# Performance work log

Hardware: AMD Instinct MI355X
Metric: run time of the kernel (lower is better)

The kernel has to match this reference:

```python
import jax, jax.numpy as jnp
import numpy as np

B, S, D, H = 2, 2048, 1024, 16
DK = D // H

def setup_inputs() -> dict:
    key = jax.random.key(0)
    ks = jax.random.split(key, 11)
    def lin(kw, kb):
        # torch nn.Linear init scale ~ 1/sqrt(fan_in)
        s = 1.0 / np.sqrt(D)
        W = jax.random.uniform(kw, (D, D), jnp.float32, -s, s)
        b = jax.random.uniform(kb, (D,), jnp.float32, -s, s)
        return W, b
    Wq, bq = lin(ks[0], ks[1])
    Wk, bk = lin(ks[2], ks[3])
    Wv, bv = lin(ks[4], ks[5])
    Wo, bo = lin(ks[6], ks[7])
    query = jax.random.normal(ks[8], (B, S, D), jnp.float32)
    key_t = jax.random.normal(ks[9], (B, S, D), jnp.float32)
    value = jax.random.normal(ks[10], (B, S, D), jnp.float32)
    return {"query": query, "key": key_t, "value": value,
            "Wq": Wq, "bq": bq, "Wk": Wk, "bk": bk,
            "Wv": Wv, "bv": bv, "Wo": Wo, "bo": bo}

def reference(query, key, value, Wq, bq, Wk, bk, Wv, bv, Wo, bo):
    # linear projections (torch Linear: x @ W.T + b), split heads -> (B,H,S,DK)
    def proj(x, W, b):
        y = jnp.einsum('bsd,ed->bse', x, W) + b
        return y.reshape(B, -1, H, DK).transpose(0, 2, 1, 3)
    q = proj(query, Wq, bq)
    k = proj(key, Wk, bk)
    v = proj(value, Wv, bv)
    # scaled dot-product attention, full score matrix (B,H,Sq,Sk)
    scores = jnp.einsum('bhqd,bhkd->bhqk', q, k) / jnp.sqrt(jnp.float32(DK))
    attn = jax.nn.softmax(scores, axis=-1)
    ctx = jnp.einsum('bhqk,bhkd->bhqd', attn, v)
    # merge heads and output projection; dropout is identity in eval mode
    ctx = ctx.transpose(0, 2, 1, 3).reshape(B, -1, D)
    out = jnp.einsum('bsd,ed->bse', ctx, Wo) + bo
    attn_weights = attn.mean(axis=1)  # average_weights=True -> (B,Sq,Sk)
    return (out, attn_weights)
```

## Files before the change

### kernel.cpp

```cpp
#include <hip/hip_runtime.h>

#define B_ 2
#define S_ 2048
#define D_ 1024
#define H_ 16
#define DK_ 64
#define M_ (B_ * S_)

typedef __bf16 bf16;
typedef __attribute__((ext_vector_type(8))) __bf16 bf16x8;
typedef __attribute__((ext_vector_type(4))) __bf16 bf16x4;
typedef __attribute__((ext_vector_type(4))) float f32x4;

static __device__ __forceinline__ bf16x8 ld8(const bf16* p) {
    return *(const bf16x8*)p;
}

static __device__ __forceinline__ void g2l16(const void* g, void* l) {
    __builtin_amdgcn_global_load_lds(
        (const __attribute__((address_space(1))) unsigned int*)g,
        (__attribute__((address_space(3))) unsigned int*)l, 16, 0, 0);
}

__global__ __launch_bounds__(256)
void cvt_all(const float* __restrict__ xq, const float* __restrict__ xk,
             const float* __restrict__ xv, const float* __restrict__ wq,
             const float* __restrict__ wk, const float* __restrict__ wv,
             const float* __restrict__ wo, bf16* __restrict__ xqo,
             bf16* __restrict__ xko, bf16* __restrict__ xvo,
             bf16* __restrict__ wqo, bf16* __restrict__ wko,
             bf16* __restrict__ wvo, bf16* __restrict__ woo)
{
    const int bx = blockIdx.x;
    const float* s; bf16* d; size_t base;
    if (bx < 6144) {
        int a = bx >> 11;
        s = (a == 0) ? xq : (a == 1) ? xk : xv;
        d = (a == 0) ? xqo : (a == 1) ? xko : xvo;
        base = (size_t)(bx & 2047) * 2048;
    } else {
        int a = (bx - 6144) >> 9;
        s = (a == 0) ? wq : (a == 1) ? wk : (a == 2) ? wv : wo;
        d = (a == 0) ? wqo : (a == 1) ? wko : (a == 2) ? wvo : woo;
        base = (size_t)((bx - 6144) & 511) * 2048;
    }
    size_t i = base + (size_t)threadIdx.x * 8;
    f32x4 a4 = *(const f32x4*)(s + i);
    f32x4 b4 = *(const f32x4*)(s + i + 4);
    bf16x8 r;
    r[0]=(bf16)a4[0]; r[1]=(bf16)a4[1]; r[2]=(bf16)a4[2]; r[3]=(bf16)a4[3];
    r[4]=(bf16)b4[0]; r[5]=(bf16)b4[1]; r[6]=(bf16)b4[2]; r[7]=(bf16)b4[3];
    *(bf16x8*)(d + i) = r;
}

__global__ __launch_bounds__(256)
void gemm128(const bf16* __restrict__ A, const bf16* __restrict__ W,
             const float* __restrict__ bias, void* __restrict__ out,
             int a_headsplit, int out_mode, float scale)
{
    const int m0 = blockIdx.x * 128, n0 = blockIdx.y * 128;
    const int tid = threadIdx.x;
    const int wv = tid >> 6, lane = tid & 63, quad = lane >> 4, l16 = lane & 15;
    const int wr = (wv >> 1) * 64, wc = (wv & 1) * 64;

    __shared__ bf16 As[128 * 32];
    __shared__ bf16 Bs[128 * 32];

    f32x4 acc[4][4];
#pragma unroll
    for (int i = 0; i < 4; ++i)
#pragma unroll
        for (int j = 0; j < 4; ++j) acc[i][j] = f32x4{0.f, 0.f, 0.f, 0.f};

    const int srow = tid >> 2;
    const int scol = (tid & 3) * 8;

    for (int k0 = 0; k0 < D_; k0 += 32) {
        bf16x8 av[2], bw[2];
#pragma unroll
        for (int c = 0; c < 2; ++c) {
            const int row = c * 64 + srow;
            const int k   = k0 + scol;
            const bf16* ap;
            if (a_headsplit) {
                int m = m0 + row, bb = m >> 11, ss = m & (S_ - 1);
                int hh = k >> 6, dd = k & (DK_ - 1);
                ap = A + (((size_t)(bb * H_ + hh) * S_ + ss) * DK_ + dd);
            } else {
                ap = A + (size_t)(m0 + row) * D_ + k;
            }
            av[c] = ld8(ap);
            bw[c] = ld8(W + (size_t)(n0 + row) * D_ + k);
        }
        __syncthreads();
#pragma unroll
        for (int c = 0; c < 2; ++c) {
            const int e = c * 2048 + tid * 8;
            *(bf16x8*)(As + e) = av[c];
            *(bf16x8*)(Bs + e) = bw[c];
        }
        __syncthreads();

        bf16x8 af[4], bfr[4];
#pragma unroll
        for (int i = 0; i < 4; ++i)
            af[i] = *(const bf16x8*)(As + (wr + i*16 + l16) * 32 + quad * 8);
#pragma unroll
        for (int j = 0; j < 4; ++j)
            bfr[j] = *(const bf16x8*)(Bs + (wc + j*16 + l16) * 32 + quad * 8);
#pragma unroll
        for (int i = 0; i < 4; ++i)
#pragma unroll
            for (int j = 0; j < 4; ++j)
                acc[i][j] = __builtin_amdgcn_mfma_f32_16x16x32_bf16(
                    af[i], bfr[j], acc[i][j], 0, 0, 0);
    }

#pragma unroll
    for (int i = 0; i < 4; ++i)
#pragma unroll
        for (int j = 0; j < 4; ++j) {
            const int nn = n0 + wc + j*16 + l16;
            const float bvv = bias[nn];
            const int mm0 = m0 + wr + i*16 + quad*4;
            if (out_mode == 2) {
                bf16x4 pk;
#pragma unroll
                for (int r = 0; r < 4; ++r)
                    pk[r] = (bf16)((acc[i][j][r] + bvv) * scale);
                int bb = mm0 >> 11, ss = mm0 & (S_ - 1);
                int hh = nn >> 6,  dd = nn & (DK_ - 1);
                *(bf16x4*)((bf16*)out +
                    ((size_t)(bb * H_ + hh) * DK_ + dd) * S_ + ss) = pk;
            } else {
#pragma unroll
                for (int r = 0; r < 4; ++r) {
                    const int mm = mm0 + r;
                    float v = (acc[i][j][r] + bvv) * scale;
                    if (out_mode == 1) {
                        ((float*)out)[(size_t)mm * D_ + nn] = v;
                    } else {
                        int bb = mm >> 11, ss = mm & (S_ - 1);
                        int hh = nn >> 6, dd = nn & (DK_ - 1);
                        ((bf16*)out)[((size_t)(bb * H_ + hh) * S_ + ss) * DK_ + dd] = (bf16)v;
                    }
                }
            }
        }
}

__global__ __launch_bounds__(256)
void attn_ctx(const bf16* __restrict__ Q, const bf16* __restrict__ K,
              const bf16* __restrict__ Vt, float* __restrict__ Li,
              bf16* __restrict__ ctxOut)
{
    const int bid = blockIdx.x;
    const int l   = (bid & 7) * 128 + (bid >> 3);
    const int q0  = (l & 31) * 64;
    const int h   = (l >> 5) & 15;
    const int b   = l >> 9;

    const int tid = threadIdx.x;
    const int wv = tid >> 6, lane = tid & 63, quad = lane >> 4, l16 = lane & 15;

    __shared__ bf16 Kl[2][2048];
    __shared__ bf16 Vl[2][2048];

    const size_t hb = (size_t)(b * H_ + h) * S_;
    const int qw = q0 + wv * 16;

    bf16x8 qf0, qf1;
    {
        const bf16* qrow = Q + (hb + qw + l16) * DK_;
        qf0 = ld8(qrow + quad*8);
        qf1 = ld8(qrow + 32 + quad*8);
    }
    const bf16* Kb  = K  + hb * DK_;
    const bf16* Vtb = Vt + hb * DK_;

    f32x4 cacc[4];
#pragma unroll
    for (int db = 0; db < 4; ++db) cacc[db] = f32x4{0.f,0.f,0.f,0.f};
    float lsum = 0.f;

    const int kj = wv*8 + (lane >> 3);
    const int koff = (((lane & 7) ^ (lane >> 3)) << 4);
    const int vd = wv*16 + (lane >> 2);
    const int voff = (((lane & 3) ^ ((lane >> 2) & 3)) << 4);

    const char* Kbc = (const char*)Kb;
    const char* Vbc = (const char*)Vtb;

#define STAGE(jc, buf)                                                       \
    do {                                                                     \
        g2l16(Kbc + ((size_t)(jc) * 32 + kj) * 128 + koff,                   \
              &Kl[buf][wv * 512]);                                           \
        g2l16(Vbc + (size_t)vd * (S_ * 2) + (size_t)(jc) * 64 + voff,        \
              &Vl[buf][wv * 512]);                                           \
    } while (0)

    STAGE(0, 0);
    __syncthreads();

    int cur = 0;
    const int swk = (l16 & 7) << 4;
    const int swv = (l16 & 3) << 4;
    for (int jc = 0; jc < 64; ++jc) {
        STAGE((jc + 1) & 63, cur ^ 1);

        const char* kb = (const char*)&Kl[cur][0];
        const char* vb = (const char*)&Vl[cur][0];
        bf16x8 kf0a = *(const bf16x8*)(kb + l16*128 + ((quad*16) ^ swk));
        bf16x8 kf0b = *(const bf16x8*)(kb + l16*128 + ((64 + quad*16) ^ swk));
        bf16x8 kf1a = *(const bf16x8*)(kb + (16+l16)*128 + ((quad*16) ^ swk));
        bf16x8 kf1b = *(const bf16x8*)(kb + (16+l16)*128 + ((64 + quad*16) ^ swk));

        f32x4 z0 = {0.f,0.f,0.f,0.f}, z1 = {0.f,0.f,0.f,0.f};
        z0 = __builtin_amdgcn_mfma_f32_16x16x32_bf16(kf0a, qf0, z0, 0, 0, 0);
        f32x4 s0 = __builtin_amdgcn_mfma_f32_16x16x32_bf16(kf0b, qf1, z0, 0, 0, 0);
        z1 = __builtin_amdgcn_mfma_f32_16x16x32_bf16(kf1a, qf0, z1, 0, 0, 0);
        f32x4 s1 = __builtin_amdgcn_mfma_f32_16x16x32_bf16(kf1b, qf1, z1, 0, 0, 0);

        float e0 = __builtin_amdgcn_exp2f(fminf(s0[0], 86.f));
        float e1 = __builtin_amdgcn_exp2f(fminf(s0[1], 86.f));
        float e2 = __builtin_amdgcn_exp2f(fminf(s0[2], 86.f));
        float e3 = __builtin_amdgcn_exp2f(fminf(s0[3], 86.f));
        float e4 = __builtin_amdgcn_exp2f(fminf(s1[0], 86.f));
        float e5 = __builtin_amdgcn_exp2f(fminf(s1[1], 86.f));
        float e6 = __builtin_amdgcn_exp2f(fminf(s1[2], 86.f));
        float e7 = __builtin_amdgcn_exp2f(fminf(s1[3], 86.f));
        lsum += ((e0 + e1) + (e2 + e3)) + ((e4 + e5) + (e6 + e7));
        bf16x8 pa;
        pa[0]=(bf16)e0; pa[1]=(bf16)e1; pa[2]=(bf16)e2; pa[3]=(bf16)e3;
        pa[4]=(bf16)e4; pa[5]=(bf16)e5; pa[6]=(bf16)e6; pa[7]=(bf16)e7;

#pragma unroll
        for (int db = 0; db < 4; ++db) {
            const int d = db*16 + l16;
            bf16x4 vlo = *(const bf16x4*)(vb + d*64 + ((quad*8) ^ swv));
            bf16x4 vhi = *(const bf16x4*)(vb + d*64 + (((32 + quad*8)) ^ swv));
            bf16x8 va = __builtin_shufflevector(vlo, vhi, 0,1,2,3,4,5,6,7);
            cacc[db] = __builtin_amdgcn_mfma_f32_16x16x32_bf16(
                va, pa, cacc[db], 0, 0, 0);
        }

        __syncthreads();
        cur ^= 1;
    }
#undef STAGE

    lsum += __shfl_xor(lsum, 16);
    lsum += __shfl_xor(lsum, 32);
    const float linv = 1.0f / fmaxf(lsum, 1e-30f);
    if (lane < 16) Li[hb + qw + lane] = lsum;

#pragma unroll
    for (int db = 0; db < 4; ++db) {
        bf16x4 pk;
#pragma unroll
        for (int r = 0; r < 4; ++r) pk[r] = (bf16)(cacc[db][r] * linv);
        *(bf16x4*)(ctxOut + (hb + qw + l16) * DK_ + db*16 + quad*4) = pk;
    }
}

__global__ __launch_bounds__(256)
void attn_weights(const bf16* __restrict__ Q, const bf16* __restrict__ K,
                  const float* __restrict__ Li, float* __restrict__ attnOut)
{
    const int bid = blockIdx.x;
    const int l   = (bid & 7) * 64 + (bid >> 3);
    const int q0  = (l & 31) * 64;
    const int b   = (l >> 5) & 1;
    const int j0  = (l >> 6) * 256;

    const int tid = threadIdx.x;
    const int wv = tid >> 6, lane = tid & 63, quad = lane >> 4, l16 = lane & 15;

    __shared__ float linv[H_][64];
#pragma unroll
    for (int i = 0; i < 4; ++i) {
        int idx = tid * 4 + i;
        int hh = idx >> 6, row = idx & 63;
        linv[hh][row] = (1.0f / H_) /
            fmaxf(Li[(size_t)(b * H_ + hh) * S_ + q0 + row], 1e-30f);
    }
    __syncthreads();

    f32x4 asum[4][4];
#pragma unroll
    for (int qt = 0; qt < 4; ++qt)
#pragma unroll
        for (int t = 0; t < 4; ++t) asum[qt][t] = f32x4{0.f,0.f,0.f,0.f};

    for (int h = 0; h < H_; ++h) {
        const size_t hb = (size_t)(b * H_ + h) * S_;
        bf16x8 qf[4][2];
        float lv[4];
#pragma unroll
        for (int qt = 0; qt < 4; ++qt) {
            const bf16* qrow = Q + (hb + q0 + qt*16 + l16) * DK_;
            qf[qt][0] = ld8(qrow + quad*8);
            qf[qt][1] = ld8(qrow + 32 + quad*8);
            lv[qt] = linv[h][qt*16 + l16];
        }
        const bf16* Kb = K + hb * DK_;
#pragma unroll
        for (int t = 0; t < 4; ++t) {
            const int jl = j0 + wv*64 + t*16;
            const bf16* krow = Kb + (size_t)(jl + l16) * DK_;
            bf16x8 kfa = ld8(krow + quad*8), kfb = ld8(krow + 32 + quad*8);
#pragma unroll
            for (int qt = 0; qt < 4; ++qt) {
                f32x4 z = {0.f,0.f,0.f,0.f};
                z = __builtin_amdgcn_mfma_f32_16x16x32_bf16(kfa, qf[qt][0], z, 0, 0, 0);
                f32x4 s = __builtin_amdgcn_mfma_f32_16x16x32_bf16(kfb, qf[qt][1], z, 0, 0, 0);
#pragma unroll
                for (int r = 0; r < 4; ++r)
                    asum[qt][t][r] += __builtin_amdgcn_exp2f(fminf(s[r], 86.f)) * lv[qt];
            }
        }
    }
#pragma unroll
    for (int qt = 0; qt < 4; ++qt)
#pragma unroll
        for (int t = 0; t < 4; ++t)
            *(f32x4*)(attnOut + ((size_t)b * S_ + q0 + qt*16 + l16) * S_
                      + j0 + wv*64 + t*16 + quad*4) = asum[qt][t];
}

extern "C" void kernel_launch(void* const* d_in, const int* in_sizes, int n_in,
                              void* d_out, int out_size, void* d_ws, size_t ws_size,
                              hipStream_t stream)
{
    (void)in_sizes; (void)n_in; (void)out_size; (void)ws_size;

    const float* query = (const float*)d_in[0];
    const float* key_t = (const float*)d_in[1];
    const float* value = (const float*)d_in[2];
    const float* Wq = (const float*)d_in[3];
    const float* bq = (const float*)d_in[4];
    const float* Wk = (const float*)d_in[5];
    const float* bk = (const float*)d_in[6];
    const float* Wv = (const float*)d_in[7];
    const float* bv = (const float*)d_in[8];
    const float* Wo = (const float*)d_in[9];
    const float* bo = (const float*)d_in[10];

    float* out     = (float*)d_out;
    float* attnOut = out + (size_t)B_ * S_ * D_;

    const size_t nX = (size_t)B_ * S_ * D_;
    const size_t nW = (size_t)D_ * D_;

    bf16* Xqb = (bf16*)d_out;
    bf16* Xkb = Xqb + nX;
    bf16* Xvb = Xkb + nX;

    bf16* Qh  = (bf16*)d_ws;
    bf16* Kh  = Qh + nX;
    bf16* VtH = Kh + nX;
    bf16* Wob = VtH + nX;
    float* Li = (float*)(Wob + nW);
    bf16* Wqb = (bf16*)(Li + (size_t)B_ * H_ * S_);
    bf16* Wkb = Wqb + nW;
    bf16* Wvb = Wkb + nW;
    bf16* CtxH = Wqb;

    cvt_all<<<8192, 256, 0, stream>>>(query, key_t, value, Wq, Wk, Wv, Wo,
                                      Xqb, Xkb, Xvb, Wqb, Wkb, Wvb, Wob);
    dim3 gg(M_/128, D_/128);
    gemm128<<<gg, 256, 0, stream>>>(Xqb, Wqb, bq, Qh, 0, 0, 0.18033688011112042f);
    gemm128<<<gg, 256, 0, stream>>>(Xkb, Wkb, bk, Kh, 0, 0, 1.0f);
    gemm128<<<gg, 256, 0, stream>>>(Xvb, Wvb, bv, VtH, 0, 2, 1.0f);
    attn_ctx    <<<1024, 256, 0, stream>>>(Qh, Kh, VtH, Li, CtxH);
    attn_weights<<<512, 256, 0, stream>>>(Qh, Kh, Li, attnOut);
    gemm128<<<gg, 256, 0, stream>>>(CtxH, Wob, bo, out, 1, 1, 1.0f);
}
```

Before: 377.1 us.

## Double attention key-chunk size and interleave V-transpose layout for 16B loads

The attention kernel now processes 64 keys per iteration instead of 32, doubling the LDS K/V buffers and halving the number of loop iterations and block barriers. The V-transposed projection epilogue writes 8-element bf16 vectors with an interleaved sequence order (pairs of 16-row tiles), so the attention kernel can read V with full 16-byte swizzled loads instead of two 8-byte loads. The added LDS and registers per block may reduce occupancy, and the permuted V layout must match the P fragment ordering exactly.

```diff
diff --git a/kernel.cpp b/kernel.cpp
--- a/kernel.cpp
+++ b/kernel.cpp
@@ -116,23 +116,35 @@
                     af[i], bfr[j], acc[i][j], 0, 0, 0);
     }
 
-#pragma unroll
-    for (int i = 0; i < 4; ++i)
+    if (out_mode == 2) {
 #pragma unroll
         for (int j = 0; j < 4; ++j) {
             const int nn = n0 + wc + j*16 + l16;
             const float bvv = bias[nn];
-            const int mm0 = m0 + wr + i*16 + quad*4;
-            if (out_mode == 2) {
-                bf16x4 pk;
-#pragma unroll
-                for (int r = 0; r < 4; ++r)
-                    pk[r] = (bf16)((acc[i][j][r] + bvv) * scale);
-                int bb = mm0 >> 11, ss = mm0 & (S_ - 1);
-                int hh = nn >> 6,  dd = nn & (DK_ - 1);
-                *(bf16x4*)((bf16*)out +
-                    ((size_t)(bb * H_ + hh) * DK_ + dd) * S_ + ss) = pk;
-            } else {
+            int hh = nn >> 6, dd = nn & (DK_ - 1);
+#pragma unroll
+            for (int ip = 0; ip < 2; ++ip) {
+                const int mlo = m0 + wr + 32*ip + quad*4;
+                int bb = mlo >> 11, sl = mlo & (S_ - 1);
+                int g0 = (sl & ~31) + ((sl & 15) << 1);
+                bf16x8 pk;
+#pragma unroll
+                for (int r = 0; r < 4; ++r) {
+                    pk[2*r]   = (bf16)((acc[2*ip  ][j][r] + bvv) * scale);
+                    pk[2*r+1] = (bf16)((acc[2*ip+1][j][r] + bvv) * scale);
+                }
+                *(bf16x8*)((bf16*)out +
+                    ((size_t)(bb * H_ + hh) * DK_ + dd) * S_ + g0) = pk;
+            }
+        }
+    } else {
+#pragma unroll
+        for (int i = 0; i < 4; ++i)
+#pragma unroll
+            for (int j = 0; j < 4; ++j) {
+                const int nn = n0 + wc + j*16 + l16;
+                const float bvv = bias[nn];
+                const int mm0 = m0 + wr + i*16 + quad*4;
 #pragma unroll
                 for (int r = 0; r < 4; ++r) {
                     const int mm = mm0 + r;
@@ -146,7 +158,7 @@
                     }
                 }
             }
-        }
+    }
 }
 
 __global__ __launch_bounds__(256)
@@ -163,8 +175,8 @@
     const int tid = threadIdx.x;
     const int wv = tid >> 6, lane = tid & 63, quad = lane >> 4, l16 = lane & 15;
 
-    __shared__ bf16 Kl[2][2048];
-    __shared__ bf16 Vl[2][2048];
+    __shared__ bf16 Kl[2][4096];
+    __shared__ bf16 Vl[2][4096];
 
     const size_t hb = (size_t)(b * H_ + h) * S_;
     const int qw = q0 + wv * 16;
@@ -175,73 +187,79 @@
         qf0 = ld8(qrow + quad*8);
         qf1 = ld8(qrow + 32 + quad*8);
     }
-    const bf16* Kb  = K  + hb * DK_;
-    const bf16* Vtb = Vt + hb * DK_;
+    const char* Kbc = (const char*)(K  + hb * DK_);
+    const char* Vbc = (const char*)(Vt + hb * DK_);
 
     f32x4 cacc[4];
 #pragma unroll
     for (int db = 0; db < 4; ++db) cacc[db] = f32x4{0.f,0.f,0.f,0.f};
     float lsum = 0.f;
 
-    const int kj = wv*8 + (lane >> 3);
-    const int koff = (((lane & 7) ^ (lane >> 3)) << 4);
-    const int vd = wv*16 + (lane >> 2);
-    const int voff = (((lane & 3) ^ ((lane >> 2) & 3)) << 4);
-
-    const char* Kbc = (const char*)Kb;
-    const char* Vbc = (const char*)Vtb;
-
-#define STAGE(jc, buf)                                                       \
-    do {                                                                     \
-        g2l16(Kbc + ((size_t)(jc) * 32 + kj) * 128 + koff,                   \
-              &Kl[buf][wv * 512]);                                           \
-        g2l16(Vbc + (size_t)vd * (S_ * 2) + (size_t)(jc) * 64 + voff,        \
-              &Vl[buf][wv * 512]);                                           \
+    const int rbK  = wv * 16;
+    const int rlan = lane >> 3;
+    const int off  = (((lane & 7) ^ rlan) << 4);
+
+#define STAGE(jc, buf)                                                        \
+    do {                                                                      \
+        const size_t jb = (size_t)(jc) * 64;                                  \
+        g2l16(Kbc + (jb + rbK + rlan) * 128 + off,      &Kl[buf][rbK*64]);    \
+        g2l16(Kbc + (jb + rbK + 8 + rlan) * 128 + off,  &Kl[buf][(rbK+8)*64]);\
+        g2l16(Vbc + (size_t)(rbK + rlan) * (S_*2) + jb*2 + off,               \
+              &Vl[buf][rbK*64]);                                              \
+        g2l16(Vbc + (size_t)(rbK + 8 + rlan) * (S_*2) + jb*2 + off,           \
+              &Vl[buf][(rbK+8)*64]);                                          \
     } while (0)
 
     STAGE(0, 0);
     __syncthreads();
 
     int cur = 0;
-    const int swk = (l16 & 7) << 4;
-    const int swv = (l16 & 3) << 4;
-    for (int jc = 0; jc < 64; ++jc) {
-        STAGE((jc + 1) & 63, cur ^ 1);
+    const int sw = (l16 & 7) << 4;
+    for (int jc = 0; jc < 32; ++jc) {
+        STAGE((jc + 1) & 31, cur ^ 1);
 
         const char* kb = (const char*)&Kl[cur][0];
         const char* vb = (const char*)&Vl[cur][0];
-        bf16x8 kf0a = *(const bf16x8*)(kb + l16*128 + ((quad*16) ^ swk));
-        bf16x8 kf0b = *(const bf16x8*)(kb + l16*128 + ((64 + quad*16) ^ swk));
-        bf16x8 kf1a = *(const bf16x8*)(kb + (16+l16)*128 + ((quad*16) ^ swk));
-        bf16x8 kf1b = *(const bf16x8*)(kb + (16+l16)*128 + ((64 + quad*16) ^ swk));
-
-        f32x4 z0 = {0.f,0.f,0.f,0.f}, z1 = {0.f,0.f,0.f,0.f};
-        z0 = __builtin_amdgcn_mfma_f32_16x16x32_bf16(kf0a, qf0, z0, 0, 0, 0);
-        f32x4 s0 = __builtin_amdgcn_mfma_f32_16x16x32_bf16(kf0b, qf1, z0, 0, 0, 0);
-        z1 = __builtin_amdgcn_mfma_f32_16x16x32_bf16(kf1a, qf0, z1, 0, 0, 0);
-        f32x4 s1 = __builtin_amdgcn_mfma_f32_16x16x32_bf16(kf1b, qf1, z1, 0, 0, 0);
-
-        float e0 = __builtin_amdgcn_exp2f(fminf(s0[0], 86.f));
-        float e1 = __builtin_amdgcn_exp2f(fminf(s0[1], 86.f));
-        float e2 = __builtin_amdgcn_exp2f(fminf(s0[2], 86.f));
-        float e3 = __builtin_amdgcn_exp2f(fminf(s0[3], 86.f));
-        float e4 = __builtin_amdgcn_exp2f(fminf(s1[0], 86.f));
-        float e5 = __builtin_amdgcn_exp2f(fminf(s1[1], 86.f));
-        float e6 = __builtin_amdgcn_exp2f(fminf(s1[2], 86.f));
-        float e7 = __builtin_amdgcn_exp2f(fminf(s1[3], 86.f));
-        lsum += ((e0 + e1) + (e2 + e3)) + ((e4 + e5) + (e6 + e7));
-        bf16x8 pa;
-        pa[0]=(bf16)e0; pa[1]=(bf16)e1; pa[2]=(bf16)e2; pa[3]=(bf16)e3;
-        pa[4]=(bf16)e4; pa[5]=(bf16)e5; pa[6]=(bf16)e6; pa[7]=(bf16)e7;
+
+        f32x4 sc[4];
+#pragma unroll
+        for (int t = 0; t < 4; ++t) {
+            const char* kr = kb + (t*16 + l16) * 128;
+            bf16x8 ka = *(const bf16x8*)(kr + ((quad*16) ^ sw));
+            bf16x8 kbv = *(const bf16x8*)(kr + ((64 + quad*16) ^ sw));
+            f32x4 z = {0.f,0.f,0.f,0.f};
+            z = __builtin_amdgcn_mfma_f32_16x16x32_bf16(ka, qf0, z, 0, 0, 0);
+            sc[t] = __builtin_amdgcn_mfma_f32_16x16x32_bf16(kbv, qf1, z, 0, 0, 0);
+        }
+
+        float ex[4][4];
+#pragma unroll
+        for (int t = 0; t < 4; ++t)
+#pragma unroll
+            for (int r = 0; r < 4; ++r)
+                ex[t][r] = __builtin_amdgcn_exp2f(fminf(sc[t][r], 86.f));
+#pragma unroll
+        for (int t = 0; t < 4; ++t)
+            lsum += (ex[t][0] + ex[t][1]) + (ex[t][2] + ex[t][3]);
+
+        bf16x8 pa0, pa1;
+#pragma unroll
+        for (int r = 0; r < 4; ++r) {
+            pa0[2*r]   = (bf16)ex[0][r];
+            pa0[2*r+1] = (bf16)ex[1][r];
+            pa1[2*r]   = (bf16)ex[2][r];
+            pa1[2*r+1] = (bf16)ex[3][r];
+        }
 
 #pragma unroll
         for (int db = 0; db < 4; ++db) {
-            const int d = db*16 + l16;
-            bf16x4 vlo = *(const bf16x4*)(vb + d*64 + ((quad*8) ^ swv));
-            bf16x4 vhi = *(const bf16x4*)(vb + d*64 + (((32 + quad*8)) ^ swv));
-            bf16x8 va = __builtin_shufflevector(vlo, vhi, 0,1,2,3,4,5,6,7);
+            const char* vr = vb + (db*16 + l16) * 128;
+            bf16x8 va0 = *(const bf16x8*)(vr + ((quad*16) ^ sw));
+            bf16x8 va1 = *(const bf16x8*)(vr + ((64 + quad*16) ^ sw));
             cacc[db] = __builtin_amdgcn_mfma_f32_16x16x32_bf16(
-                va, pa, cacc[db], 0, 0, 0);
+                va0, pa0, cacc[db], 0, 0, 0);
+            cacc[db] = __builtin_amdgcn_mfma_f32_16x16x32_bf16(
+                va1, pa1, cacc[db], 0, 0, 0);
         }
 
         __syncthreads();
```

Measured after the change: 342.7 us. 9.1% less time.
